# Optimization experiments

Hardware: AMD Instinct MI355X
Metric: run time of the kernel (lower is better)

Reference implementation:

```python
import jax, jax.numpy as jnp
import numpy as np

N = 50000          # nodes
E = 800000         # edges
D_IN = 768         # LM embedding dim (hardcoded in SimpleHGN first conv)
H = 128            # hidden_dim
REL_DIM = 32       # hardcoded rel_dim
N_REL = 3          # n_relations
BETA = 0.05        # SimpleHGN_att_res
NEG_SLOPE = 0.2    # LeakyReLU in attention


def setup_inputs() -> dict:
    key = jax.random.key(0)
    ks = jax.random.split(key, 16)
    s = 0.05  # param init scale
    return {
        'x': jax.random.normal(ks[0], (N, D_IN), jnp.float32),
        'edge_index': jax.random.randint(ks[1], (2, E), 0, N, dtype=jnp.int64),
        'edge_type': jax.random.randint(ks[2], (E,), 0, N_REL, dtype=jnp.int64),
        'W0': jax.random.normal(ks[3], (D_IN, H), jnp.float32) * s,
        'Wr0': jax.random.normal(ks[4], (REL_DIM, H), jnp.float32) * s,
        'a0': jax.random.normal(ks[5], (3 * H, 1), jnp.float32) * s,
        'rel0': jax.random.normal(ks[6], (N_REL, REL_DIM), jnp.float32) * s,
        'W1': jax.random.normal(ks[7], (H, H), jnp.float32) * s,
        'Wr1': jax.random.normal(ks[8], (REL_DIM, H), jnp.float32) * s,
        'a1': jax.random.normal(ks[9], (3 * H, 1), jnp.float32) * s,
        'rel1': jax.random.normal(ks[10], (N_REL, REL_DIM), jnp.float32) * s,
        'pool_w': jax.random.normal(ks[11], (H, H), jnp.float32) * s,
        'pool_b': jnp.zeros((H,), jnp.float32),
        'out_w': jax.random.normal(ks[12], (H, 2), jnp.float32) * s,
        'out_b': jnp.zeros((2,), jnp.float32),
    }


def _hgn_conv(x, src, dst, et, W, Wr, a, rel, pre_alpha):
    """One SimpleHGNConv layer. Returns (ELU(aggregated), alpha detached)."""
    h = x @ W                                   # [N, H]
    r = rel[et] @ Wr                            # [E, H] edge-type embedding
    aw = a[:, 0]
    a_i, a_j, a_r = aw[:h.shape[1]], aw[h.shape[1]:2 * h.shape[1]], aw[2 * h.shape[1]:]
    # logits = leaky_relu(cat(h_i, h_j, r) @ a) computed without [E,3H] concat
    node_i = h @ a_i                            # [N]
    node_j = h @ a_j                            # [N]
    logit = jax.nn.leaky_relu(node_i[dst] + node_j[src] + r @ a_r, NEG_SLOPE)  # [E]
    # segment softmax over destination node neighborhoods (PyG softmax, +1e-16)
    m = jax.ops.segment_max(logit, dst, num_segments=N)
    e = jnp.exp(logit - m[dst])
    ssum = jax.ops.segment_sum(e, dst, num_segments=N)
    alpha = e / (ssum[dst] + 1e-16)             # [E]
    if pre_alpha is not None:
        alpha = alpha * (1.0 - BETA) + pre_alpha * BETA
    msg = h[src] * alpha[:, None]               # [E, H]
    out = jax.ops.segment_sum(msg, dst, num_segments=N)  # [N, H]
    return jax.nn.elu(out), jax.lax.stop_gradient(alpha)


def reference(x, edge_index, edge_type, W0, Wr0, a0, rel0, W1, Wr1, a1, rel1,
              pool_w, pool_b, out_w, out_b):
    src, dst = edge_index[0], edge_index[1]     # x_j = source, x_i = target
    h, alpha = _hgn_conv(x, src, dst, edge_type, W0, Wr0, a0, rel0, None)
    h, alpha = _hgn_conv(h, src, dst, edge_type, W1, Wr1, a1, rel1, alpha)
    # dropout is identity in eval; activation = relu per config
    h = jax.nn.relu(h @ pool_w + pool_b)
    return h @ out_w + out_b                    # [N, 2]
```

## Files before the change

### kernel.cpp

```cpp
#include <hip/hip_runtime.h>
#include <hip/hip_fp16.h>
#include <cstdint>
#include <cstddef>

#define N_NODES 50000
#define N_EDGES 800000
#define DIN_    768
#define H_DIM   128
#define N_REL   3
#define BETA_F  0.05f
#define SLOPE_F 0.2f

static inline int cdiv(int a, int b) { return (a + b - 1) / b; }

typedef __attribute__((ext_vector_type(8))) short bf16x8;
typedef __attribute__((ext_vector_type(8))) unsigned short u16x8;
typedef __attribute__((ext_vector_type(4))) float f32x4;

__device__ __forceinline__ unsigned short f2bf(float f) {
  unsigned u = __builtin_bit_cast(unsigned, f);
  unsigned r = (u + 0x7fffu + ((u >> 16) & 1u)) >> 16;
  return (unsigned short)r;
}
__device__ __forceinline__ float bf2f(unsigned short h) {
  unsigned u = ((unsigned)h) << 16;
  return __builtin_bit_cast(float, u);
}

#define GLOAD_LDS16(g, s) __builtin_amdgcn_global_load_lds( \
    (const __attribute__((address_space(1))) void*)(g),      \
    (__attribute__((address_space(3))) void*)(s), 16, 0, 0)

__global__ void k_count(const int* __restrict__ dst, int* __restrict__ deg, int E) {
  int e = blockIdx.x * blockDim.x + threadIdx.x;
  if (e < E) atomicAdd(&deg[dst[e]], 1);
}

__global__ __launch_bounds__(256) void k_scan1(const int* __restrict__ deg,
                                               int* __restrict__ part, int n) {
  __shared__ int wsum[4];
  int i = blockIdx.x * 256 + threadIdx.x;
  int lane = threadIdx.x & 63, w = threadIdx.x >> 6;
  int v = (i < n) ? deg[i] : 0;
  #pragma unroll
  for (int d = 32; d > 0; d >>= 1) v += __shfl_xor(v, d);
  if (lane == 0) wsum[w] = v;
  __syncthreads();
  if (threadIdx.x == 0) part[blockIdx.x] = wsum[0] + wsum[1] + wsum[2] + wsum[3];
}

__global__ __launch_bounds__(256) void k_scan2(int* __restrict__ part,
                                               int* __restrict__ off, int nb, int n) {
  __shared__ int sh[256];
  int t = threadIdx.x;
  int v = (t < nb) ? part[t] : 0;
  int incl = v;
  sh[t] = incl;
  __syncthreads();
  #pragma unroll
  for (int d = 1; d < 256; d <<= 1) {
    int u = (t >= d) ? sh[t - d] : 0;
    __syncthreads();
    sh[t] += u;
    __syncthreads();
  }
  incl = sh[t];
  if (t < nb) part[t] = incl - v;
  if (t == nb - 1) off[n] = incl;
}

__global__ __launch_bounds__(256) void k_scan3(const int* __restrict__ deg,
                                               const int* __restrict__ part,
                                               int* __restrict__ off,
                                               int* __restrict__ cur, int n) {
  __shared__ int wsum[4];
  int i = blockIdx.x * 256 + threadIdx.x;
  int lane = threadIdx.x & 63, w = threadIdx.x >> 6;
  int v = (i < n) ? deg[i] : 0;
  int incl = v;
  #pragma unroll
  for (int d = 1; d < 64; d <<= 1) {
    int u = __shfl_up(incl, d);
    if (lane >= d) incl += u;
  }
  if (lane == 63) wsum[w] = incl;
  __syncthreads();
  int woff = 0;
  #pragma unroll
  for (int k = 0; k < 4; ++k) woff += (k < w) ? wsum[k] : 0;
  int ex = incl - v + woff + part[blockIdx.x];
  if (i < n) { off[i] = ex; cur[i] = ex; }
}

__global__ void k_fill(const int* __restrict__ dst, int* __restrict__ cur,
                       int* __restrict__ csr, int E) {
  int e = blockIdx.x * blockDim.x + threadIdx.x;
  if (e < E) {
    int p = atomicAdd(&cur[dst[e]], 1);
    csr[p] = e;
  }
}

__global__ __launch_bounds__(128) void k_relscore(const float* __restrict__ rel,
                                                  const float* __restrict__ Wr,
                                                  const float* __restrict__ a,
                                                  float* __restrict__ rs) {
  __shared__ float red[128];
  int k = threadIdx.x;
  for (int t = 0; t < N_REL; ++t) {
    float p = 0.f;
    #pragma unroll
    for (int j = 0; j < 32; ++j) p += rel[t * 32 + j] * Wr[j * H_DIM + k];
    red[k] = p * a[2 * H_DIM + k];
    __syncthreads();
    for (int s = 64; s > 0; s >>= 1) {
      if (k < s) red[k] += red[k + s];
      __syncthreads();
    }
    if (k == 0) rs[t] = red[0];
    __syncthreads();
  }
}

__global__ void k_prep(const float* __restrict__ W, int K,
                       short* __restrict__ th, short* __restrict__ tl) {
  int id = blockIdx.x * 256 + threadIdx.x;
  if (id >= K * 128) return;
  int k = id >> 7, c = id & 127;
  float w = W[id];
  unsigned short h = f2bf(w);
  unsigned short l = f2bf(w - bf2f(h));
  int kt = k >> 6;
  int g = (k >> 3) & 7;
  int j = k & 7;
  int p = g ^ (c & 7);
  size_t pos = ((size_t)(kt * 128 + c) << 6) + (p << 3) + j;
  th[pos] = (short)h;
  tl[pos] = (short)l;
}

template <bool BIASRELU, bool W16>
__global__ __launch_bounds__(256, 3) void k_gemm_mfma(const float* __restrict__ A,
                                                      const short* __restrict__ Bswh,
                                                      const short* __restrict__ Bswl,
                                                      const float* __restrict__ bias,
                                                      float* __restrict__ C,
                                                      __half* __restrict__ C16,
                                                      int n, int K) {
  __shared__ __align__(16) char Asm[16384];
  __shared__ __align__(16) char Bhs[16384];
  __shared__ __align__(16) char Bls[16384];
  int t = threadIdx.x;
  int l = t & 63, wid = t >> 6;
  int wr = wid >> 1, wc = wid & 1;
  int lr = l & 15, lk = l >> 4;
  int row0 = blockIdx.x * 64;

  f32x4 acc[2][4];
  #pragma unroll
  for (int m = 0; m < 2; ++m)
    #pragma unroll
    for (int nn = 0; nn < 4; ++nn) acc[m][nn] = (f32x4)(0.f);

  const int nt = K >> 6;

  int a_r[4], a_gl[4];
  #pragma unroll
  for (int i = 0; i < 4; ++i) {
    int id = (wid * 4 + i) * 64 + l;
    int r = id >> 4, s = id & 15;
    int p32 = s >> 1, b = s & 1;
    a_r[i] = r;
    a_gl[i] = (((p32 ^ (r & 7)) << 1) | b);
  }

  for (int it = 0; it < nt; ++it) {
    int k0 = it << 6;
    #pragma unroll
    for (int i = 0; i < 4; ++i) {
      int gr = row0 + a_r[i]; if (gr >= n) gr = n - 1;
      const float* src = A + (size_t)gr * K + k0 + a_gl[i] * 4;
      GLOAD_LDS16(src, Asm + (wid * 4 + i) * 1024);
    }
    const short* bh_t = Bswh + (size_t)it * 8192;
    const short* bl_t = Bswl + (size_t)it * 8192;
    #pragma unroll
    for (int i = 0; i < 4; ++i) {
      int id = (wid * 4 + i) * 64 + l;
      GLOAD_LDS16(bh_t + id * 8, Bhs + (wid * 4 + i) * 1024);
    }
    #pragma unroll
    for (int i = 0; i < 4; ++i) {
      int id = (wid * 4 + i) * 64 + l;
      GLOAD_LDS16(bl_t + id * 8, Bls + (wid * 4 + i) * 1024);
    }
    __syncthreads();

    #pragma unroll
    for (int kk = 0; kk < 2; ++kk) {
      int q = kk * 4 + lk;
      bf16x8 ah[2], al[2];
      #pragma unroll
      for (int m = 0; m < 2; ++m) {
        int r = wr * 32 + m * 16 + lr;
        const char* ap = Asm + r * 256 + ((q ^ (r & 7)) << 5);
        float4 f0 = *(const float4*)ap;
        float4 f1 = *(const float4*)(ap + 16);
        float ff[8] = {f0.x, f0.y, f0.z, f0.w, f1.x, f1.y, f1.z, f1.w};
        u16x8 hv, lv;
        #pragma unroll
        for (int j = 0; j < 8; ++j) {
          unsigned u = __builtin_bit_cast(unsigned, ff[j]);
          unsigned short h = (unsigned short)(u >> 16);
          hv[j] = h;
          lv[j] = f2bf(ff[j] - bf2f(h));
        }
        ah[m] = __builtin_bit_cast(bf16x8, hv);
        al[m] = __builtin_bit_cast(bf16x8, lv);
      }
      bf16x8 bh[4], bl[4];
      #pragma unroll
      for (int nn = 0; nn < 4; ++nn) {
        int c = wc * 64 + nn * 16 + lr;
        int p = q ^ (c & 7);
        bh[nn] = *(const bf16x8*)(Bhs + c * 128 + p * 16);
        bl[nn] = *(const bf16x8*)(Bls + c * 128 + p * 16);
      }
      #pragma unroll
      for (int m = 0; m < 2; ++m)
        #pragma unroll
        for (int nn = 0; nn < 4; ++nn) {
          acc[m][nn] = __builtin_amdgcn_mfma_f32_16x16x32_bf16(ah[m], bh[nn], acc[m][nn], 0, 0, 0);
          acc[m][nn] = __builtin_amdgcn_mfma_f32_16x16x32_bf16(ah[m], bl[nn], acc[m][nn], 0, 0, 0);
          acc[m][nn] = __builtin_amdgcn_mfma_f32_16x16x32_bf16(al[m], bh[nn], acc[m][nn], 0, 0, 0);
        }
    }
    __syncthreads();
  }

  #pragma unroll
  for (int m = 0; m < 2; ++m) {
    int rbase = row0 + wr * 32 + m * 16 + lk * 4;
    #pragma unroll
    for (int nn = 0; nn < 4; ++nn) {
      int c = wc * 64 + nn * 16 + lr;
      #pragma unroll
      for (int q = 0; q < 4; ++q) {
        int r = rbase + q;
        if (r < n) {
          float v = acc[m][nn][q];
          if (BIASRELU) {
            v += bias[c];
            v = v > 0.f ? v : 0.f;
          }
          C[(size_t)r * 128 + c] = v;
          if (W16) C16[(size_t)r * 128 + c] = __float2half(v);
        }
      }
    }
  }
}

__global__ __launch_bounds__(256) void k_scores(const float* __restrict__ h,
                                                const float* __restrict__ a,
                                                float* __restrict__ ni,
                                                float* __restrict__ nj, int n) {
  int lane = threadIdx.x & 63;
  int w = threadIdx.x >> 6;
  int row = blockIdx.x * 4 + w;
  if (row >= n) return;
  float2 v = ((const float2*)(h + (size_t)row * H_DIM))[lane];
  float2 ai = ((const float2*)a)[lane];
  float2 aj = ((const float2*)(a + H_DIM))[lane];
  float si = v.x * ai.x + v.y * ai.y;
  float sj = v.x * aj.x + v.y * aj.y;
  #pragma unroll
  for (int d = 32; d > 0; d >>= 1) {
    si += __shfl_xor(si, d);
    sj += __shfl_xor(sj, d);
  }
  if (lane == 0) { ni[row] = si; nj[row] = sj; }
}

__global__ void k_logit(const int* __restrict__ src, const int* __restrict__ dst,
                        const int* __restrict__ et,
                        const float* __restrict__ ni, const float* __restrict__ nj,
                        const float* __restrict__ rs,
                        float* __restrict__ logit, int E) {
  int e = blockIdx.x * blockDim.x + threadIdx.x;
  if (e >= E) return;
  float v = ni[dst[e]] + nj[src[e]] + rs[et[e]];
  logit[e] = v > 0.f ? v : SLOPE_F * v;
}

template <int LAYER>
__global__ __launch_bounds__(128) void k_aggregate(const int* __restrict__ off,
                                                   const int* __restrict__ csr,
                                                   const int* __restrict__ src,
                                                   const float* __restrict__ logit,
                                                   const __half* __restrict__ h16,
                                                   float* __restrict__ alpha_io,
                                                   float* __restrict__ hout, int n) {
  __shared__ float l_red[2];
  __shared__ float l_alpha[128];
  __shared__ int   l_src[128];
  int nid = blockIdx.x;
  int t = threadIdx.x;
  int lane = t & 63;
  int w = t >> 6;
  int start = off[nid];
  int deg = off[nid + 1] - start;
  float hv = 0.f;
  if (deg > 0) {
    float m = -INFINITY;
    for (int k = t; k < deg; k += 128) m = fmaxf(m, logit[csr[start + k]]);
    #pragma unroll
    for (int d = 32; d > 0; d >>= 1) m = fmaxf(m, __shfl_xor(m, d));
    if (lane == 0) l_red[w] = m;
    __syncthreads();
    m = fmaxf(l_red[0], l_red[1]);
    __syncthreads();
    float s = 0.f;
    for (int k = t; k < deg; k += 128) s += expf(logit[csr[start + k]] - m);
    #pragma unroll
    for (int d = 32; d > 0; d >>= 1) s += __shfl_xor(s, d);
    if (lane == 0) l_red[w] = s;
    __syncthreads();
    float denom = l_red[0] + l_red[1] + 1e-16f;
    for (int base = 0; base < deg; base += 128) {
      int kk = base + t;
      if (kk < deg) {
        int e = csr[start + kk];
        float al = expf(logit[e] - m) / denom;
        if (LAYER == 1) {
          al = al * (1.f - BETA_F) + BETA_F * alpha_io[e];
        } else {
          alpha_io[e] = al;
        }
        l_alpha[t] = al;
        l_src[t] = src[e];
      }
      __syncthreads();
      int cnt = deg - base; if (cnt > 128) cnt = 128;
      #pragma unroll 4
      for (int k = 0; k < cnt; ++k)
        hv += l_alpha[k] * __half2float(h16[(size_t)l_src[k] * H_DIM + t]);
      __syncthreads();
    }
  }
  hout[(size_t)nid * H_DIM + t] = hv > 0.f ? hv : expm1f(hv);
}

__global__ __launch_bounds__(256) void k_out(const float* __restrict__ P,
                                             const float* __restrict__ ow,
                                             const float* __restrict__ ob,
                                             float* __restrict__ out, int n) {
  int lane = threadIdx.x & 63;
  int w = threadIdx.x >> 6;
  int row = blockIdx.x * 4 + w;
  if (row >= n) return;
  float2 v  = ((const float2*)(P + (size_t)row * H_DIM))[lane];
  float2 w0 = ((const float2*)ow)[2 * lane];
  float2 w1 = ((const float2*)ow)[2 * lane + 1];
  float s0 = v.x * w0.x + v.y * w1.x;
  float s1 = v.x * w0.y + v.y * w1.y;
  #pragma unroll
  for (int d = 32; d > 0; d >>= 1) {
    s0 += __shfl_xor(s0, d);
    s1 += __shfl_xor(s1, d);
  }
  if (lane == 0) {
    out[row * 2]     = s0 + ob[0];
    out[row * 2 + 1] = s1 + ob[1];
  }
}

extern "C" void kernel_launch(void* const* d_in, const int* in_sizes, int n_in,
                              void* d_out, int out_size, void* d_ws, size_t ws_size,
                              hipStream_t stream) {
  const float* x      = (const float*)d_in[0];
  const int*   ei     = (const int*)d_in[1];
  const int*   et     = (const int*)d_in[2];
  const float* W0     = (const float*)d_in[3];
  const float* Wr0    = (const float*)d_in[4];
  const float* a0     = (const float*)d_in[5];
  const float* rel0   = (const float*)d_in[6];
  const float* W1     = (const float*)d_in[7];
  const float* Wr1    = (const float*)d_in[8];
  const float* a1     = (const float*)d_in[9];
  const float* rel1   = (const float*)d_in[10];
  const float* pool_w = (const float*)d_in[11];
  const float* pool_b = (const float*)d_in[12];
  const float* out_w  = (const float*)d_in[13];
  const float* out_b  = (const float*)d_in[14];

  const int* src = ei;
  const int* dst = ei + N_EDGES;

  char* p = (char*)d_ws;
  auto take = [&](size_t bytes) {
    char* r = p;
    p += (bytes + 511) & ~(size_t)511;
    return r;
  };
  int*   deg    = (int*)take((size_t)N_NODES * 4);
  int*   off    = (int*)take((size_t)(N_NODES + 1) * 4);
  int*   cur    = (int*)take((size_t)N_NODES * 4);
  int*   part   = (int*)take((size_t)256 * 4);
  int*   csr    = (int*)take((size_t)N_EDGES * 4);
  float* logit  = (float*)take((size_t)N_EDGES * 4);
  float* alpha0 = (float*)take((size_t)N_EDGES * 4);
  float* ni     = (float*)take((size_t)N_NODES * 4);
  float* nj     = (float*)take((size_t)N_NODES * 4);
  float* rs     = (float*)take(256);
  short* wt0h   = (short*)take((size_t)DIN_ * 128 * 2);
  short* wt0l   = (short*)take((size_t)DIN_ * 128 * 2);
  short* wt1h   = (short*)take((size_t)128 * 128 * 2);
  short* wt1l   = (short*)take((size_t)128 * 128 * 2);
  short* wph    = (short*)take((size_t)128 * 128 * 2);
  short* wpl    = (short*)take((size_t)128 * 128 * 2);
  float* big1   = (float*)take((size_t)N_NODES * H_DIM * 4);
  float* big2   = (float*)take((size_t)N_NODES * H_DIM * 4);
  __half* h16   = (__half*)take((size_t)N_NODES * H_DIM * 2);

  const int EB = cdiv(N_EDGES, 256);
  const int GB = cdiv(N_NODES, 64);
  const int SB = cdiv(N_NODES, 256);

  hipMemsetAsync(deg, 0, (size_t)N_NODES * 4, stream);
  k_count<<<EB, 256, 0, stream>>>(dst, deg, N_EDGES);
  k_scan1<<<SB, 256, 0, stream>>>(deg, part, N_NODES);
  k_scan2<<<1, 256, 0, stream>>>(part, off, SB, N_NODES);
  k_scan3<<<SB, 256, 0, stream>>>(deg, part, off, cur, N_NODES);
  k_fill<<<EB, 256, 0, stream>>>(dst, cur, csr, N_EDGES);

  k_prep<<<cdiv(DIN_ * 128, 256), 256, 0, stream>>>(W0, DIN_, wt0h, wt0l);
  k_prep<<<cdiv(128 * 128, 256), 256, 0, stream>>>(W1, 128, wt1h, wt1l);
  k_prep<<<cdiv(128 * 128, 256), 256, 0, stream>>>(pool_w, 128, wph, wpl);

  k_relscore<<<1, 128, 0, stream>>>(rel0, Wr0, a0, rs);
  k_gemm_mfma<false, true><<<GB, 256, 0, stream>>>(x, wt0h, wt0l, nullptr, big1, h16, N_NODES, DIN_);
  k_scores<<<cdiv(N_NODES, 4), 256, 0, stream>>>(big1, a0, ni, nj, N_NODES);
  k_logit<<<EB, 256, 0, stream>>>(src, dst, et, ni, nj, rs, logit, N_EDGES);
  k_aggregate<0><<<N_NODES, 128, 0, stream>>>(off, csr, src, logit, h16, alpha0, big2, N_NODES);

  k_relscore<<<1, 128, 0, stream>>>(rel1, Wr1, a1, rs);
  k_gemm_mfma<false, true><<<GB, 256, 0, stream>>>(big2, wt1h, wt1l, nullptr, big1, h16, N_NODES, 128);
  k_scores<<<cdiv(N_NODES, 4), 256, 0, stream>>>(big1, a1, ni, nj, N_NODES);
  k_logit<<<EB, 256, 0, stream>>>(src, dst, et, ni, nj, rs, logit, N_EDGES);
  k_aggregate<1><<<N_NODES, 128, 0, stream>>>(off, csr, src, logit, h16, alpha0, big2, N_NODES);

  k_gemm_mfma<true, false><<<GB, 256, 0, stream>>>(big2, wph, wpl, pool_b, big1, nullptr, N_NODES, 128);
  k_out<<<cdiv(N_NODES, 4), 256, 0, stream>>>(big1, out_w, out_b, (float*)d_out, N_NODES);
}
```

Measured before the change: 395.1 us.

## Fuse node scores into GEMM epilogue and compute logits inside aggregation via sorted CSR

The node attention scores (h·a_i, h·a_j) are now reduced in the GEMM epilogue with shuffles and shared memory, which removes the separate k_scores pass over h. The per-edge logit kernel is dropped and logits are recomputed on the fly inside the aggregation from dst-sorted src/edge-type arrays written during CSR fill. Alpha is also stored in sorted order, which removes the indirect csr lookups. In exchange, logits are recomputed on each pass past the first 128 edges, and the fill kernel writes two arrays instead of one.

```diff
diff --git a/kernel.cpp b/kernel.cpp
--- a/kernel.cpp
+++ b/kernel.cpp
@@ -92,12 +92,14 @@
   if (i < n) { off[i] = ex; cur[i] = ex; }
 }
 
-__global__ void k_fill(const int* __restrict__ dst, int* __restrict__ cur,
-                       int* __restrict__ csr, int E) {
+__global__ void k_fill(const int* __restrict__ dst, const int* __restrict__ src,
+                       const int* __restrict__ et, int* __restrict__ cur,
+                       int* __restrict__ src_s, int* __restrict__ et_s, int E) {
   int e = blockIdx.x * blockDim.x + threadIdx.x;
   if (e < E) {
     int p = atomicAdd(&cur[dst[e]], 1);
-    csr[p] = e;
+    src_s[p] = src[e];
+    et_s[p] = et[e];
   }
 }
 
@@ -139,17 +141,21 @@
   tl[pos] = (short)l;
 }
 
-template <bool BIASRELU, bool W16>
+template <bool BIASRELU, bool W16, bool SCORES>
 __global__ __launch_bounds__(256, 3) void k_gemm_mfma(const float* __restrict__ A,
                                                       const short* __restrict__ Bswh,
                                                       const short* __restrict__ Bswl,
                                                       const float* __restrict__ bias,
+                                                      const float* __restrict__ av,
                                                       float* __restrict__ C,
                                                       __half* __restrict__ C16,
+                                                      float* __restrict__ ni,
+                                                      float* __restrict__ nj,
                                                       int n, int K) {
   __shared__ __align__(16) char Asm[16384];
   __shared__ __align__(16) char Bhs[16384];
   __shared__ __align__(16) char Bls[16384];
+  __shared__ float nip[2][64], njp[2][64];
   int t = threadIdx.x;
   int l = t & 63, wid = t >> 6;
   int wr = wid >> 1, wc = wid & 1;
@@ -238,6 +244,19 @@
     __syncthreads();
   }
 
+  float avi[4], avj[4];
+  if (SCORES) {
+    #pragma unroll
+    for (int nn = 0; nn < 4; ++nn) {
+      int c = wc * 64 + nn * 16 + lr;
+      avi[nn] = av[c];
+      avj[nn] = av[H_DIM + c];
+    }
+  }
+  float pi[8], pj[8];
+  #pragma unroll
+  for (int i = 0; i < 8; ++i) { pi[i] = 0.f; pj[i] = 0.f; }
+
   #pragma unroll
   for (int m = 0; m < 2; ++m) {
     int rbase = row0 + wr * 32 + m * 16 + lk * 4;
@@ -247,8 +266,12 @@
       #pragma unroll
       for (int q = 0; q < 4; ++q) {
         int r = rbase + q;
+        float v = acc[m][nn][q];
+        if (SCORES) {
+          pi[m * 4 + q] += v * avi[nn];
+          pj[m * 4 + q] += v * avj[nn];
+        }
         if (r < n) {
-          float v = acc[m][nn][q];
           if (BIASRELU) {
             v += bias[c];
             v = v > 0.f ? v : 0.f;
@@ -259,47 +282,46 @@
       }
     }
   }
-}
-
-__global__ __launch_bounds__(256) void k_scores(const float* __restrict__ h,
-                                                const float* __restrict__ a,
-                                                float* __restrict__ ni,
-                                                float* __restrict__ nj, int n) {
-  int lane = threadIdx.x & 63;
-  int w = threadIdx.x >> 6;
-  int row = blockIdx.x * 4 + w;
-  if (row >= n) return;
-  float2 v = ((const float2*)(h + (size_t)row * H_DIM))[lane];
-  float2 ai = ((const float2*)a)[lane];
-  float2 aj = ((const float2*)(a + H_DIM))[lane];
-  float si = v.x * ai.x + v.y * ai.y;
-  float sj = v.x * aj.x + v.y * aj.y;
-  #pragma unroll
-  for (int d = 32; d > 0; d >>= 1) {
-    si += __shfl_xor(si, d);
-    sj += __shfl_xor(sj, d);
-  }
-  if (lane == 0) { ni[row] = si; nj[row] = sj; }
-}
-
-__global__ void k_logit(const int* __restrict__ src, const int* __restrict__ dst,
-                        const int* __restrict__ et,
-                        const float* __restrict__ ni, const float* __restrict__ nj,
-                        const float* __restrict__ rs,
-                        float* __restrict__ logit, int E) {
-  int e = blockIdx.x * blockDim.x + threadIdx.x;
-  if (e >= E) return;
-  float v = ni[dst[e]] + nj[src[e]] + rs[et[e]];
-  logit[e] = v > 0.f ? v : SLOPE_F * v;
+
+  if (SCORES) {
+    #pragma unroll
+    for (int d = 1; d < 16; d <<= 1) {
+      #pragma unroll
+      for (int i = 0; i < 8; ++i) {
+        pi[i] += __shfl_xor(pi[i], d);
+        pj[i] += __shfl_xor(pj[i], d);
+      }
+    }
+    if (lr == 0) {
+      #pragma unroll
+      for (int m = 0; m < 2; ++m)
+        #pragma unroll
+        for (int q = 0; q < 4; ++q) {
+          int rl = wr * 32 + m * 16 + lk * 4 + q;
+          nip[wc][rl] = pi[m * 4 + q];
+          njp[wc][rl] = pj[m * 4 + q];
+        }
+    }
+    __syncthreads();
+    if (t < 64) {
+      int r = row0 + t;
+      if (r < n) {
+        ni[r] = nip[0][t] + nip[1][t];
+        nj[r] = njp[0][t] + njp[1][t];
+      }
+    }
+  }
 }
 
 template <int LAYER>
 __global__ __launch_bounds__(128) void k_aggregate(const int* __restrict__ off,
-                                                   const int* __restrict__ csr,
-                                                   const int* __restrict__ src,
-                                                   const float* __restrict__ logit,
+                                                   const int* __restrict__ src_s,
+                                                   const int* __restrict__ et_s,
+                                                   const float* __restrict__ ni,
+                                                   const float* __restrict__ nj,
+                                                   const float* __restrict__ rs,
                                                    const __half* __restrict__ h16,
-                                                   float* __restrict__ alpha_io,
+                                                   float* __restrict__ alpha_s,
                                                    float* __restrict__ hout, int n) {
   __shared__ float l_red[2];
   __shared__ float l_alpha[128];
@@ -312,16 +334,26 @@
   int deg = off[nid + 1] - start;
   float hv = 0.f;
   if (deg > 0) {
-    float m = -INFINITY;
-    for (int k = t; k < deg; k += 128) m = fmaxf(m, logit[csr[start + k]]);
+    float r0 = rs[0], r1 = rs[1], r2 = rs[2];
+    float base_i = ni[nid];
+    auto LG = [&](int k) {
+      int p = start + k;
+      int et = et_s[p];
+      float rv = et == 0 ? r0 : (et == 1 ? r1 : r2);
+      float v = base_i + nj[src_s[p]] + rv;
+      return v > 0.f ? v : SLOPE_F * v;
+    };
+    float lg0 = (t < deg) ? LG(t) : -INFINITY;
+    float m = lg0;
+    for (int k = t + 128; k < deg; k += 128) m = fmaxf(m, LG(k));
     #pragma unroll
     for (int d = 32; d > 0; d >>= 1) m = fmaxf(m, __shfl_xor(m, d));
     if (lane == 0) l_red[w] = m;
     __syncthreads();
     m = fmaxf(l_red[0], l_red[1]);
     __syncthreads();
-    float s = 0.f;
-    for (int k = t; k < deg; k += 128) s += expf(logit[csr[start + k]] - m);
+    float s = (t < deg) ? expf(lg0 - m) : 0.f;
+    for (int k = t + 128; k < deg; k += 128) s += expf(LG(k) - m);
     #pragma unroll
     for (int d = 32; d > 0; d >>= 1) s += __shfl_xor(s, d);
     if (lane == 0) l_red[w] = s;
@@ -330,15 +362,15 @@
     for (int base = 0; base < deg; base += 128) {
       int kk = base + t;
       if (kk < deg) {
-        int e = csr[start + kk];
-        float al = expf(logit[e] - m) / denom;
+        float lg = base ? LG(kk) : lg0;
+        float al = expf(lg - m) / denom;
         if (LAYER == 1) {
-          al = al * (1.f - BETA_F) + BETA_F * alpha_io[e];
+          al = al * (1.f - BETA_F) + BETA_F * alpha_s[start + kk];
         } else {
-          alpha_io[e] = al;
+          alpha_s[start + kk] = al;
         }
         l_alpha[t] = al;
-        l_src[t] = src[e];
+        l_src[t] = src_s[start + kk];
       }
       __syncthreads();
       int cnt = deg - base; if (cnt > 128) cnt = 128;
@@ -403,25 +435,25 @@
     p += (bytes + 511) & ~(size_t)511;
     return r;
   };
-  int*   deg    = (int*)take((size_t)N_NODES * 4);
-  int*   off    = (int*)take((size_t)(N_NODES + 1) * 4);
-  int*   cur    = (int*)take((size_t)N_NODES * 4);
-  int*   part   = (int*)take((size_t)256 * 4);
-  int*   csr    = (int*)take((size_t)N_EDGES * 4);
-  float* logit  = (float*)take((size_t)N_EDGES * 4);
-  float* alpha0 = (float*)take((size_t)N_EDGES * 4);
-  float* ni     = (float*)take((size_t)N_NODES * 4);
-  float* nj     = (float*)take((size_t)N_NODES * 4);
-  float* rs     = (float*)take(256);
-  short* wt0h   = (short*)take((size_t)DIN_ * 128 * 2);
-  short* wt0l   = (short*)take((size_t)DIN_ * 128 * 2);
-  short* wt1h   = (short*)take((size_t)128 * 128 * 2);
-  short* wt1l   = (short*)take((size_t)128 * 128 * 2);
-  short* wph    = (short*)take((size_t)128 * 128 * 2);
-  short* wpl    = (short*)take((size_t)128 * 128 * 2);
-  float* big1   = (float*)take((size_t)N_NODES * H_DIM * 4);
-  float* big2   = (float*)take((size_t)N_NODES * H_DIM * 4);
-  __half* h16   = (__half*)take((size_t)N_NODES * H_DIM * 2);
+  int*   deg     = (int*)take((size_t)N_NODES * 4);
+  int*   off     = (int*)take((size_t)(N_NODES + 1) * 4);
+  int*   cur     = (int*)take((size_t)N_NODES * 4);
+  int*   part    = (int*)take((size_t)256 * 4);
+  int*   src_s   = (int*)take((size_t)N_EDGES * 4);
+  int*   et_s    = (int*)take((size_t)N_EDGES * 4);
+  float* alpha_s = (float*)take((size_t)N_EDGES * 4);
+  float* ni      = (float*)take((size_t)N_NODES * 4);
+  float* nj      = (float*)take((size_t)N_NODES * 4);
+  float* rs      = (float*)take(256);
+  short* wt0h    = (short*)take((size_t)DIN_ * 128 * 2);
+  short* wt0l    = (short*)take((size_t)DIN_ * 128 * 2);
+  short* wt1h    = (short*)take((size_t)128 * 128 * 2);
+  short* wt1l    = (short*)take((size_t)128 * 128 * 2);
+  short* wph     = (short*)take((size_t)128 * 128 * 2);
+  short* wpl     = (short*)take((size_t)128 * 128 * 2);
+  float* big1    = (float*)take((size_t)N_NODES * H_DIM * 4);
+  float* big2    = (float*)take((size_t)N_NODES * H_DIM * 4);
+  __half* h16    = (__half*)take((size_t)N_NODES * H_DIM * 2);
 
   const int EB = cdiv(N_EDGES, 256);
   const int GB = cdiv(N_NODES, 64);
@@ -432,24 +464,26 @@
   k_scan1<<<SB, 256, 0, stream>>>(deg, part, N_NODES);
   k_scan2<<<1, 256, 0, stream>>>(part, off, SB, N_NODES);
   k_scan3<<<SB, 256, 0, stream>>>(deg, part, off, cur, N_NODES);
-  k_fill<<<EB, 256, 0, stream>>>(dst, cur, csr, N_EDGES);
+  k_fill<<<EB, 256, 0, stream>>>(dst, src, et, cur, src_s, et_s, N_EDGES);
 
   k_prep<<<cdiv(DIN_ * 128, 256), 256, 0, stream>>>(W0, DIN_, wt0h, wt0l);
   k_prep<<<cdiv(128 * 128, 256), 256, 0, stream>>>(W1, 128, wt1h, wt1l);
   k_prep<<<cdiv(128 * 128, 256), 256, 0, stream>>>(pool_w, 128, wph, wpl);
 
   k_relscore<<<1, 128, 0, stream>>>(rel0, Wr0, a0, rs);
-  k_gemm_mfma<false, true><<<GB, 256, 0, stream>>>(x, wt0h, wt0l, nullptr, big1, h16, N_NODES, DIN_);
-  k_scores<<<cdiv(N_NODES, 4), 256, 0, stream>>>(big1, a0, ni, nj, N_NODES);
-  k_logit<<<EB, 256, 0, stream>>>(src, dst, et, ni, nj, rs, logit, N_EDGES);
-  k_aggregate<0><<<N_NODES, 128, 0, stream>>>(off, csr, src, logit, h16, alpha0, big2, N_NODES);
+  k_gemm_mfma<false, true, true><<<GB, 256, 0, stream>>>(x, wt0h, wt0l, nullptr, a0,
+                                                         big1, h16, ni, nj, N_NODES, DIN_);
+  k_aggregate<0><<<N_NODES, 128, 0, stream>>>(off, src_s, et_s, ni, nj, rs, h16,
+                                              alpha_s, big2, N_NODES);
 
   k_relscore<<<1, 128, 0, stream>>>(rel1, Wr1, a1, rs);
-  k_gemm_mfma<false, true><<<GB, 256, 0, stream>>>(big2, wt1h, wt1l, nullptr, big1, h16, N_NODES, 128);
-  k_scores<<<cdiv(N_NODES, 4), 256, 0, stream>>>(big1, a1, ni, nj, N_NODES);
-  k_logit<<<EB, 256, 0, stream>>>(src, dst, et, ni, nj, rs, logit, N_EDGES);
-  k_aggregate<1><<<N_NODES, 128, 0, stream>>>(off, csr, src, logit, h16, alpha0, big2, N_NODES);
-
-  k_gemm_mfma<true, false><<<GB, 256, 0, stream>>>(big2, wph, wpl, pool_b, big1, nullptr, N_NODES, 128);
+  k_gemm_mfma<false, true, true><<<GB, 256, 0, stream>>>(big2, wt1h, wt1l, nullptr, a1,
+                                                         big1, h16, ni, nj, N_NODES, 128);
+  k_aggregate<1><<<N_NODES, 128, 0, stream>>>(off, src_s, et_s, ni, nj, rs, h16,
+                                              alpha_s, big2, N_NODES);
+
+  k_gemm_mfma<true, false, false><<<GB, 256, 0, stream>>>(big2, wph, wpl, pool_b, nullptr,
+                                                          big1, nullptr, nullptr, nullptr,
+                                                          N_NODES, 128);
   k_out<<<cdiv(N_NODES, 4), 256, 0, stream>>>(big1, out_w, out_b, (float*)d_out, N_NODES);
 }
```

Result: slower. 453.6 us (+14.8%).
